# Optimization experiments

Hardware: AMD Instinct MI355X
Metric: run time of the kernel (lower is better)

Reference implementation:

```python
import jax, jax.numpy as jnp
import numpy as np

B, C_IN, C_OUT = 2, 64, 64
NLAT_IN, NLON_IN = 181, 360
NLAT_OUT, NLON_OUT = 181, 360
KERNEL_SIZE = 9            # piecewise-linear basis, kernel_shape=(3,4): (3-1)*4+1
NNZ_PER = 24               # sparse neighbor entries per (kernel fn, output latitude)
NNZ = KERNEL_SIZE * NLAT_OUT * NNZ_PER


def setup_inputs() -> dict:
    key = jax.random.key(0)
    ks = jax.random.split(key, 6)
    x = jax.random.normal(ks[0], (B, C_IN, NLAT_IN, NLON_IN), jnp.float32)
    # quadrature-merged, normalized filter values (positive, O(1/support) scale)
    psi_vals = jax.random.uniform(ks[1], (NNZ,), jnp.float32) / NNZ_PER
    # structured sparse pattern: every (kernel, lat_out) pair has NNZ_PER neighbors
    psi_ker = jnp.repeat(jnp.arange(KERNEL_SIZE, dtype=jnp.int32), NLAT_OUT * NNZ_PER)
    psi_lat_out = jnp.tile(jnp.repeat(jnp.arange(NLAT_OUT, dtype=jnp.int32), NNZ_PER), KERNEL_SIZE)
    dlat = jax.random.randint(ks[2], (NNZ,), -1, 2, dtype=jnp.int32)
    psi_lat_in = jnp.clip(psi_lat_out + dlat, 0, NLAT_IN - 1)
    psi_lon_in = jax.random.randint(ks[3], (NNZ,), 0, NLON_IN, dtype=jnp.int32)
    scale = (1.0 / (C_IN * KERNEL_SIZE)) ** 0.5
    weight = scale * jax.random.normal(ks[4], (C_OUT, C_IN, KERNEL_SIZE), jnp.float32)
    bias = jnp.zeros((C_OUT,), jnp.float32)
    return dict(x=x, psi_vals=psi_vals, weight=weight, bias=bias,
                psi_ker=psi_ker, psi_lat_out=psi_lat_out,
                psi_lat_in=psi_lat_in, psi_lon_in=psi_lon_in)


def _disco_contraction(x, psi_vals, psi_ker, psi_lat_out, psi_lat_in, psi_lon_in):
    """Sparse DISCO contraction: y[b,c,k,lat_out,p] = sum_e psi_vals[e] *
    x[b,c,lat_in_e,(lon_in_e + p*pscale) % nlon_in]  for entries with (k_e, lat_out_e).
    Mirrors torch-harmonics' roll-and-sparse-bmm loop over output longitudes."""
    b, c, nlat_in, nlon_in = x.shape
    pscale = nlon_in // NLON_OUT
    xf = x.reshape(b * c, nlat_in, nlon_in)          # [BC, nlat_in, nlon_in]
    seg = psi_ker * NLAT_OUT + psi_lat_out           # [NNZ] segment id = (k, lat_out)
    nseg = KERNEL_SIZE * NLAT_OUT

    def one_shift(p):
        lon = (psi_lon_in + p * pscale) % nlon_in    # rolled longitude per entry
        g = xf[:, psi_lat_in, lon] * psi_vals        # [BC, NNZ] gather-multiply
        return jax.ops.segment_sum(g.T, seg, num_segments=nseg)  # [nseg, BC]

    ys = jax.lax.map(one_shift, jnp.arange(NLON_OUT))            # [NLON_OUT, nseg, BC]
    y = ys.transpose(1, 0, 2).reshape(KERNEL_SIZE, NLAT_OUT, NLON_OUT, b, c)
    return y.transpose(3, 4, 0, 1, 2)                # [B, C_in, K, nlat_out, nlon_out]


def reference(x, psi_vals, weight, bias, psi_ker, psi_lat_out, psi_lat_in, psi_lon_in):
    y = _disco_contraction(x, psi_vals, psi_ker, psi_lat_out, psi_lat_in, psi_lon_in)
    # groups=1: weight is [C_out, C_in, K]
    out = jnp.einsum("bckxy,fck->bfxy", y, weight)
    out = out + bias[None, :, None, None]
    return out
```

## Files before the change

kernel.cpp:

```cpp
#include <hip/hip_runtime.h>


#define NB    2
#define CIN   64
#define COUT  64
#define KS    9
#define NLAT  181
#define NLON  360
#define NPER  24

typedef _Float16 f16;
typedef _Float16 f16x8 __attribute__((ext_vector_type(8)));
typedef float    f32x4 __attribute__((ext_vector_type(4)));
typedef unsigned int u32;
typedef unsigned short u16;
typedef u32 u32x4 __attribute__((ext_vector_type(4)));

#define ROWB      46080
#define XT_BYTES  ((size_t)NB * NLAT * NLON * 64 * 2)
#define WT_BYTES  (KS * 64 * 64 * 2)
#define NMETA     (KS * NLAT * NPER)
#define XS_BYTES  (3 * ROWB)

#define U0  (NB * NLAT * 90 * 8)
#define G0  ((U0 + 255) / 256)
#define G1  ((KS * 4096 + 255) / 256)
#define G2  ((NMETA + 255) / 256)

__global__ __launch_bounds__(256) void prep_kernel(
    const float* __restrict__ x, const float* __restrict__ weight,
    const float* __restrict__ psi_vals, const int* __restrict__ psi_lat_in,
    const int* __restrict__ psi_lon_in,
    f16* __restrict__ xT, f16* __restrict__ wT, int4* __restrict__ meta)
{
    const int bid = blockIdx.x, tid = threadIdx.x;
    if (bid < G0) {
        const int u = bid * 256 + tid;
        if (u >= U0) return;
        const int ch   = u & 7;
        const int v    = u >> 3;
        const int lon4 = v % 90;
        const int w    = v / 90;
        const int lat  = w % NLAT;
        const int b    = w / NLAT;
        const int lon0 = lon4 * 4;
        const float* src = x + ((size_t)(b * CIN + ch * 8) * NLAT + lat) * NLON + lon0;
        f32x4 L[8];
#pragma unroll
        for (int j = 0; j < 8; ++j)
            L[j] = *(const f32x4*)&src[(size_t)j * NLAT * NLON];
        f16* xd = xT + ((size_t)(b * NLAT + lat) * NLON + lon0) * 64;
        const int pbase = ch ^ (lon0 & 7);
#pragma unroll
        for (int dl = 0; dl < 4; ++dl) {
            f16x8 vv;
#pragma unroll
            for (int j = 0; j < 8; ++j) vv[j] = (f16)L[j][dl];
            *(f16x8*)&xd[dl * 64 + (pbase ^ dl) * 8] = vv;
        }
        return;
    }
    if (bid < G0 + G1) {
        const int e = (bid - G0) * 256 + tid;
        if (e < KS * 4096) {
            int c = e & 63, f = (e >> 6) & 63, k = e >> 12;
            wT[e] = (f16)weight[((size_t)(f * 64 + c)) * KS + k];
        }
        return;
    }
    {
        const int e = (bid - G0 - G1) * 256 + tid;
        if (e < NMETA) {
            int lat = (e / NPER) % NLAT;
            f16 pvh = (f16)psi_vals[e];
            u32 pb = (u32)__builtin_bit_cast(u16, pvh);
            int lonb = psi_lon_in[e] << 7;
            int4 m;
            m.x = (int)((pb << 16) | pb);
            m.y = (psi_lat_in[e] - lat + 1) * ROWB + lonb;
            m.z = lonb;
            m.w = 0;
            meta[e] = m;
        }
    }
}

__global__ __launch_bounds__(768, 3) void disco_main(
    const f16* __restrict__ xT, const f16* __restrict__ wT,
    const int4* __restrict__ meta, const float* __restrict__ bias,
    float* __restrict__ out)
{
    extern __shared__ char xs[];
    const int tid  = threadIdx.x;
    const int lane = tid & 63, wave = tid >> 6;
    const int pn   = lane & 15, q = lane >> 4;
    const int half2 = blockIdx.x, lat = blockIdx.y, b = blockIdx.z;

    const int tile = half2 * 12 + wave;
    const bool act = tile < 23;
    const int p  = tile * 16 + pn;
    const int pl = p >= NLON ? p - NLON : p;
    const u32 plq  = (u32)((pl << 7) + (q << 4));
    const u32 plqm = plq - (u32)ROWB;
    const u32 thr  = (u32)((NLON - pl) << 7);

    const int rr0 = lat > 0 ? lat - 1 : 0;
    const int rr2 = lat < NLAT - 1 ? lat + 1 : NLAT - 1;

    {
        const size_t bb = (size_t)b * NLAT;
        const f16* s0 = xT + (bb + rr0) * NLON * 64;
        const f16* s1 = xT + (bb + lat) * NLON * 64;
        const f16* s2 = xT + (bb + rr2) * NLON * 64;
        for (int i = tid; i < 2880; i += 768) {
            *(f16x8*)&xs[i * 16]             = *(const f16x8*)&s0[i * 8];
            *(f16x8*)&xs[ROWB + i * 16]      = *(const f16x8*)&s1[i * 8];
            *(f16x8*)&xs[2 * ROWB + i * 16]  = *(const f16x8*)&s2[i * 8];
        }
    }
    __syncthreads();

    f32x4 D[4];
#pragma unroll
    for (int ft = 0; ft < 4; ++ft) D[ft] = (f32x4){0.f, 0.f, 0.f, 0.f};

    if (act) {
        for (int k = 0; k < KS; ++k) {
            f16x8 acc0 = (f16x8){0, 0, 0, 0, 0, 0, 0, 0};
            f16x8 acc1 = (f16x8){0, 0, 0, 0, 0, 0, 0, 0};
            const int4* mp = meta + (k * NLAT + lat) * NPER;
#pragma unroll
            for (int tg = 0; tg < NPER; tg += 4) {
                int4 m[4];
#pragma unroll
                for (int j = 0; j < 4; ++j) m[j] = mp[tg + j];

                u32 a0[4], a1[4];
#pragma unroll
                for (int j = 0; j < 4; ++j) {
                    u32 ad = ((u32)m[j].z >= thr) ? plqm : plq;
                    u32 t  = (u32)m[j].y + ad;
                    u32 a  = t ^ ((t >> 3) & 0x70u);
                    a0[j] = a;
                    a1[j] = a ^ 64u;
                }
                f16x8 xv0[4], xv1[4];
#pragma unroll
                for (int j = 0; j < 4; ++j) xv0[j] = *(const f16x8*)(xs + a0[j]);
#pragma unroll
                for (int j = 0; j < 4; ++j) xv1[j] = *(const f16x8*)(xs + a1[j]);
#pragma unroll
                for (int j = 0; j < 4; ++j) {
                    u32 pk = (u32)m[j].x;
                    u32x4 pkv = {pk, pk, pk, pk};
                    f16x8 pf = __builtin_bit_cast(f16x8, pkv);
                    acc0 += xv0[j] * pf;
                    acc1 += xv1[j] * pf;
                }
            }

            f16x8 Af0[4], Af1[4];
            const f16* wk = wT + (size_t)k * 4096 + q * 8;
#pragma unroll
            for (int ft = 0; ft < 4; ++ft) {
                Af0[ft] = *(const f16x8*)&wk[(ft * 16 + pn) * 64];
                Af1[ft] = *(const f16x8*)&wk[32 + (ft * 16 + pn) * 64];
            }
#pragma unroll
            for (int ft = 0; ft < 4; ++ft) {
                D[ft] = __builtin_amdgcn_mfma_f32_16x16x32_f16(Af0[ft], acc0, D[ft], 0, 0, 0);
                D[ft] = __builtin_amdgcn_mfma_f32_16x16x32_f16(Af1[ft], acc1, D[ft], 0, 0, 0);
            }
        }
    }

    if (act && p < NLON) {
#pragma unroll
        for (int ft = 0; ft < 4; ++ft)
#pragma unroll
            for (int r = 0; r < 4; ++r) {
                const int f = ft * 16 + q * 4 + r;
                out[((size_t)(b * COUT + f) * NLAT + lat) * NLON + p] = D[ft][r] + bias[f];
            }
    }
}

extern "C" void kernel_launch(void* const* d_in, const int* in_sizes, int n_in,
                              void* d_out, int out_size, void* d_ws, size_t ws_size,
                              hipStream_t stream) {
    const float* x          = (const float*)d_in[0];
    const float* psi_vals   = (const float*)d_in[1];
    const float* weight     = (const float*)d_in[2];
    const float* bias       = (const float*)d_in[3];
    const int*   psi_lat_in = (const int*)d_in[6];
    const int*   psi_lon_in = (const int*)d_in[7];
    float* out = (float*)d_out;

    f16*  xT   = (f16*)d_ws;
    f16*  wT   = (f16*)((char*)d_ws + XT_BYTES);
    int4* meta = (int4*)((char*)d_ws + XT_BYTES + WT_BYTES);

    (void)hipFuncSetAttribute((const void*)disco_main,
                              hipFuncAttributeMaxDynamicSharedMemorySize, XS_BYTES);

    prep_kernel<<<dim3(G0 + G1 + G2), 256, 0, stream>>>(
        x, weight, psi_vals, psi_lat_in, psi_lon_in, xT, wT, meta);
    disco_main<<<dim3(2, NLAT, NB), 768, XS_BYTES, stream>>>(
        xT, wT, meta, bias, out);
}
```

Baseline: 192.5 us.

## Quantize input to per-row int8 and dequantize in-kernel via byte permutes

Adds a scale pass that computes a per-(batch, latitude) max-abs scale and quantizes x to offset-binary int8 in place of fp16. This halves the workspace and LDS footprint, so occupancy can rise (launch bounds go from 3 to 6 blocks). The row scale is folded into the psi values stored in the metadata. Inside the gather loop, bytes are expanded to fp16 with v_perm and a magic-number bias. The cost is reduced precision, plus an extra kernel launch and another full read of x.

```diff
diff --git a/kernel.cpp b/kernel.cpp
--- a/kernel.cpp
+++ b/kernel.cpp
@@ -14,24 +14,65 @@
 typedef float    f32x4 __attribute__((ext_vector_type(4)));
 typedef unsigned int u32;
 typedef unsigned short u16;
+typedef unsigned char u8;
 typedef u32 u32x4 __attribute__((ext_vector_type(4)));
 
-#define ROWB      46080
-#define XT_BYTES  ((size_t)NB * NLAT * NLON * 64 * 2)
+#define ROWB8     23040
+#define SLOTB     23552
+#define XT8_BYTES ((size_t)NB * NLAT * ROWB8)
 #define WT_BYTES  (KS * 64 * 64 * 2)
 #define NMETA     (KS * NLAT * NPER)
-#define XS_BYTES  (3 * ROWB)
+#define META_BYTES ((size_t)NMETA * 16)
+#define XS_BYTES  (3 * SLOTB)
 
 #define U0  (NB * NLAT * 90 * 8)
 #define G0  ((U0 + 255) / 256)
 #define G1  ((KS * 4096 + 255) / 256)
 #define G2  ((NMETA + 255) / 256)
 
+#define SEL_LO 0x05010400u
+#define SEL_HI 0x05030402u
+
+__device__ __forceinline__ u32 bperm(u32 s0, u32 s1, u32 sel) {
+#if __has_builtin(__builtin_amdgcn_perm)
+    return __builtin_amdgcn_perm(s0, s1, sel);
+#else
+    u32 r = 0;
+#pragma unroll
+    for (int i = 0; i < 4; ++i) {
+        u32 code = (sel >> (8 * i)) & 0xffu;
+        u32 byte = code < 4 ? (s1 >> (8 * code)) : (s0 >> (8 * (code - 4)));
+        r |= (byte & 0xffu) << (8 * i);
+    }
+    return r;
+#endif
+}
+
+__global__ __launch_bounds__(256) void scale_kernel(
+    const float* __restrict__ x, float* __restrict__ srow)
+{
+    __shared__ float red[256];
+    const int lat = blockIdx.x, b = blockIdx.y, tid = threadIdx.x;
+    float mx = 0.f;
+    for (int c = 0; c < CIN; ++c) {
+        const float* row = x + ((size_t)(b * CIN + c) * NLAT + lat) * NLON;
+        for (int l = tid; l < NLON; l += 256)
+            mx = fmaxf(mx, fabsf(row[l]));
+    }
+    red[tid] = mx;
+    __syncthreads();
+    for (int s = 128; s > 0; s >>= 1) {
+        if (tid < s) red[tid] = fmaxf(red[tid], red[tid + s]);
+        __syncthreads();
+    }
+    if (tid == 0) srow[b * NLAT + lat] = fmaxf(red[0], 1e-20f) * (1.f / 127.f);
+}
+
 __global__ __launch_bounds__(256) void prep_kernel(
     const float* __restrict__ x, const float* __restrict__ weight,
     const float* __restrict__ psi_vals, const int* __restrict__ psi_lat_in,
-    const int* __restrict__ psi_lon_in,
-    f16* __restrict__ xT, f16* __restrict__ wT, int4* __restrict__ meta)
+    const int* __restrict__ psi_lon_in, const float* __restrict__ srow,
+    u8* __restrict__ xT8, f16* __restrict__ wT, int4* __restrict__ meta)
 {
     const int bid = blockIdx.x, tid = threadIdx.x;
     if (bid < G0) {
@@ -44,19 +85,29 @@
         const int lat  = w % NLAT;
         const int b    = w / NLAT;
         const int lon0 = lon4 * 4;
+        const float qs = 1.0f / srow[b * NLAT + lat];
         const float* src = x + ((size_t)(b * CIN + ch * 8) * NLAT + lat) * NLON + lon0;
         f32x4 L[8];
 #pragma unroll
         for (int j = 0; j < 8; ++j)
             L[j] = *(const f32x4*)&src[(size_t)j * NLAT * NLON];
-        f16* xd = xT + ((size_t)(b * NLAT + lat) * NLON + lon0) * 64;
-        const int pbase = ch ^ (lon0 & 7);
+        u8* xrow = xT8 + (size_t)(b * NLAT + lat) * ROWB8;
+        const u32 ub = (u32)((ch & 3) * 16 + (ch >> 2) * 8);
 #pragma unroll
         for (int dl = 0; dl < 4; ++dl) {
-            f16x8 vv;
-#pragma unroll
-            for (int j = 0; j < 8; ++j) vv[j] = (f16)L[j][dl];
-            *(f16x8*)&xd[dl * 64 + (pbase ^ dl) * 8] = vv;
+            u32 d0 = 0, d1 = 0;
+#pragma unroll
+            for (int j = 0; j < 8; ++j) {
+                float qf = __builtin_rintf(L[j][dl] * qs);
+                qf = fminf(fmaxf(qf, -127.f), 127.f);
+                u32 uq = (u32)(int)(qf + 128.f);
+                if (j < 4) d0 |= uq << (8 * j);
+                else       d1 |= uq << (8 * (j - 4));
+            }
+            u32 uoff = (u32)((lon0 + dl) * 64) + ub;
+            u32 a = uoff ^ ((uoff >> 3) & 0x70u);
+            uint2 st = {d0, d1};
+            *(uint2*)(xrow + a) = st;
         }
         return;
     }
@@ -72,21 +123,23 @@
         const int e = (bid - G0 - G1) * 256 + tid;
         if (e < NMETA) {
             int lat = (e / NPER) % NLAT;
-            f16 pvh = (f16)psi_vals[e];
-            u32 pb = (u32)__builtin_bit_cast(u16, pvh);
-            int lonb = psi_lon_in[e] << 7;
+            int li  = psi_lat_in[e];
+            float psi = psi_vals[e];
+            u32 h0 = (u32)__builtin_bit_cast(u16, (f16)(psi * srow[0 * NLAT + li]));
+            u32 h1 = (u32)__builtin_bit_cast(u16, (f16)(psi * srow[1 * NLAT + li]));
+            int lonb = psi_lon_in[e] << 6;
             int4 m;
-            m.x = (int)((pb << 16) | pb);
-            m.y = (psi_lat_in[e] - lat + 1) * ROWB + lonb;
+            m.x = (int)(h0 | (h0 << 16));
+            m.y = (li - lat + 1) * SLOTB + lonb;
             m.z = lonb;
-            m.w = 0;
+            m.w = (int)(h1 | (h1 << 16));
             meta[e] = m;
         }
     }
 }
 
-__global__ __launch_bounds__(768, 3) void disco_main(
-    const f16* __restrict__ xT, const f16* __restrict__ wT,
+__global__ __launch_bounds__(768, 6) void disco_main(
+    const u8* __restrict__ xT8, const f16* __restrict__ wT,
     const int4* __restrict__ meta, const float* __restrict__ bias,
     float* __restrict__ out)
 {
@@ -100,22 +153,22 @@
     const bool act = tile < 23;
     const int p  = tile * 16 + pn;
     const int pl = p >= NLON ? p - NLON : p;
-    const u32 plq  = (u32)((pl << 7) + (q << 4));
-    const u32 plqm = plq - (u32)ROWB;
-    const u32 thr  = (u32)((NLON - pl) << 7);
+    const u32 plq  = (u32)((pl << 6) + (q << 4));
+    const u32 plqm = plq - (u32)ROWB8;
+    const u32 thr  = (u32)((NLON - pl) << 6);
 
     const int rr0 = lat > 0 ? lat - 1 : 0;
     const int rr2 = lat < NLAT - 1 ? lat + 1 : NLAT - 1;
 
     {
         const size_t bb = (size_t)b * NLAT;
-        const f16* s0 = xT + (bb + rr0) * NLON * 64;
-        const f16* s1 = xT + (bb + lat) * NLON * 64;
-        const f16* s2 = xT + (bb + rr2) * NLON * 64;
-        for (int i = tid; i < 2880; i += 768) {
-            *(f16x8*)&xs[i * 16]             = *(const f16x8*)&s0[i * 8];
-            *(f16x8*)&xs[ROWB + i * 16]      = *(const f16x8*)&s1[i * 8];
-            *(f16x8*)&xs[2 * ROWB + i * 16]  = *(const f16x8*)&s2[i * 8];
+        const char* s0 = (const char*)xT8 + (bb + rr0) * ROWB8;
+        const char* s1 = (const char*)xT8 + (bb + lat) * ROWB8;
+        const char* s2 = (const char*)xT8 + (bb + rr2) * ROWB8;
+        for (int i = tid; i < 1440; i += 768) {
+            *(u32x4*)&xs[i * 16]             = *(const u32x4*)&s0[i * 16];
+            *(u32x4*)&xs[SLOTB + i * 16]     = *(const u32x4*)&s1[i * 16];
+            *(u32x4*)&xs[2 * SLOTB + i * 16] = *(const u32x4*)&s2[i * 16];
         }
     }
     __syncthreads();
@@ -123,6 +176,11 @@
     f32x4 D[4];
 #pragma unroll
     for (int ft = 0; ft < 4; ++ft) D[ft] = (f32x4){0.f, 0.f, 0.f, 0.f};
+
+    const u32 C64 = 0x64646464u;
+    const u32 BB  = 0xE480E480u;
+    const f16x8 B8 = __builtin_bit_cast(f16x8, (u32x4){BB, BB, BB, BB});
+    const bool bsel = (b != 0);
 
     if (act) {
         for (int k = 0; k < KS; ++k) {
@@ -130,32 +188,38 @@
             f16x8 acc1 = (f16x8){0, 0, 0, 0, 0, 0, 0, 0};
             const int4* mp = meta + (k * NLAT + lat) * NPER;
 #pragma unroll
-            for (int tg = 0; tg < NPER; tg += 4) {
-                int4 m[4];
-#pragma unroll
-                for (int j = 0; j < 4; ++j) m[j] = mp[tg + j];
-
-                u32 a0[4], a1[4];
-#pragma unroll
-                for (int j = 0; j < 4; ++j) {
+            for (int tg = 0; tg < NPER; tg += 8) {
+                int4 m[8];
+#pragma unroll
+                for (int j = 0; j < 8; ++j) m[j] = mp[tg + j];
+
+                u32 a[8];
+#pragma unroll
+                for (int j = 0; j < 8; ++j) {
                     u32 ad = ((u32)m[j].z >= thr) ? plqm : plq;
                     u32 t  = (u32)m[j].y + ad;
-                    u32 a  = t ^ ((t >> 3) & 0x70u);
-                    a0[j] = a;
-                    a1[j] = a ^ 64u;
+                    a[j]   = t ^ ((t >> 3) & 0x70u);
                 }
-                f16x8 xv0[4], xv1[4];
-#pragma unroll
-                for (int j = 0; j < 4; ++j) xv0[j] = *(const f16x8*)(xs + a0[j]);
-#pragma unroll
-                for (int j = 0; j < 4; ++j) xv1[j] = *(const f16x8*)(xs + a1[j]);
-#pragma unroll
-                for (int j = 0; j < 4; ++j) {
-                    u32 pk = (u32)m[j].x;
-                    u32x4 pkv = {pk, pk, pk, pk};
-                    f16x8 pf = __builtin_bit_cast(f16x8, pkv);
-                    acc0 += xv0[j] * pf;
-                    acc1 += xv1[j] * pf;
+                u32x4 xv[8];
+#pragma unroll
+                for (int j = 0; j < 8; ++j)
+                    xv[j] = *(const u32x4*)(xs + a[j]);
+#pragma unroll
+                for (int j = 0; j < 8; ++j) {
+                    const u32 mm = bsel ? (u32)m[j].w : (u32)m[j].x;
+                    const f16x8 mh = __builtin_bit_cast(f16x8, (u32x4){mm, mm, mm, mm});
+                    u32 p0 = bperm(C64, xv[j][0], SEL_LO);
+                    u32 p1 = bperm(C64, xv[j][0], SEL_HI);
+                    u32 p2 = bperm(C64, xv[j][1], SEL_LO);
+                    u32 p3 = bperm(C64, xv[j][1], SEL_HI);
+                    f16x8 v0 = __builtin_bit_cast(f16x8, (u32x4){p0, p1, p2, p3});
+                    acc0 += mh * (v0 + B8);
+                    u32 p4 = bperm(C64, xv[j][2], SEL_LO);
+                    u32 p5 = bperm(C64, xv[j][2], SEL_HI);
+                    u32 p6 = bperm(C64, xv[j][3], SEL_LO);
+                    u32 p7 = bperm(C64, xv[j][3], SEL_HI);
+                    f16x8 v1 = __builtin_bit_cast(f16x8, (u32x4){p4, p5, p6, p7});
+                    acc1 += mh * (v1 + B8);
                 }
             }
 
@@ -196,15 +260,17 @@
     const int*   psi_lon_in = (const int*)d_in[7];
     float* out = (float*)d_out;
 
-    f16*  xT   = (f16*)d_ws;
-    f16*  wT   = (f16*)((char*)d_ws + XT_BYTES);
-    int4* meta = (int4*)((char*)d_ws + XT_BYTES + WT_BYTES);
+    u8*    xT8  = (u8*)d_ws;
+    f16*   wT   = (f16*)((char*)d_ws + XT8_BYTES);
+    int4*  meta = (int4*)((char*)d_ws + XT8_BYTES + WT_BYTES);
+    float* srow = (float*)((char*)d_ws + XT8_BYTES + WT_BYTES + META_BYTES);
 
     (void)hipFuncSetAttribute((const void*)disco_main,
                               hipFuncAttributeMaxDynamicSharedMemorySize, XS_BYTES);
 
+    scale_kernel<<<dim3(NLAT, NB), 256, 0, stream>>>(x, srow);
     prep_kernel<<<dim3(G0 + G1 + G2), 256, 0, stream>>>(
-        x, weight, psi_vals, psi_lat_in, psi_lon_in, xT, wT, meta);
+        x, weight, psi_vals, psi_lat_in, psi_lon_in, srow, xT8, wT, meta);
     disco_main<<<dim3(2, NLAT, NB), 768, XS_BYTES, stream>>>(
-        xT, wT, meta, bias, out);
-}
+        xT8, wT, meta, bias, out);
+}
```

Result: slower. 461.0 us (+139.5%).
